# Optimization experiments

Hardware: AMD Instinct MI355X
Metric: run time of the kernel (lower is better)

The kernel has to match this reference:

```python
import jax, jax.numpy as jnp
import numpy as np

N_NODES = 10000
N_EDGES = 160000
IN_CH = 256
HID = 128
HEADS = 8
OUT_CH = 32
NEG_SLOPE = 0.2  # PyG GATv2Conv default


def setup_inputs() -> dict:
    key = jax.random.key(0)
    ks = jax.random.split(key, 12)
    x = jax.random.normal(ks[0], (N_NODES, IN_CH), dtype=jnp.float32)
    edge_index = jax.random.randint(ks[1], (2, N_EDGES), 0, N_NODES, dtype=jnp.int32)
    s1 = 1.0 / np.sqrt(IN_CH)
    s2 = 1.0 / np.sqrt(HEADS * HID)
    return {
        "x": x,
        "edge_index": edge_index,
        # conv1: GATv2Conv(256 -> 128, heads=8, concat=True)
        "W1_l": jax.random.normal(ks[2], (IN_CH, HEADS * HID), dtype=jnp.float32) * s1,
        "W1_r": jax.random.normal(ks[3], (IN_CH, HEADS * HID), dtype=jnp.float32) * s1,
        "att1": jax.random.normal(ks[4], (HEADS, HID), dtype=jnp.float32) * s1,
        "b1": jnp.zeros((HEADS * HID,), dtype=jnp.float32),
        # conv2: GATv2Conv(1024 -> 32, heads=1, concat=False)
        "W2_l": jax.random.normal(ks[5], (HEADS * HID, OUT_CH), dtype=jnp.float32) * s2,
        "W2_r": jax.random.normal(ks[6], (HEADS * HID, OUT_CH), dtype=jnp.float32) * s2,
        "att2": jax.random.normal(ks[7], (1, OUT_CH), dtype=jnp.float32) * s2,
        "b2": jnp.zeros((OUT_CH,), dtype=jnp.float32),
    }


def _gatv2_conv(x, src, dst, W_l, W_r, att, bias, heads, out_ch, concat):
    """PyG GATv2Conv (inference): e_ij = att . LeakyReLU(Wl x_j + Wr x_i),
    segment-softmax over incoming edges per dst node, scatter-add of Wl x_j."""
    n = x.shape[0]
    xl = (x @ W_l).reshape(n, heads, out_ch)  # source transform [N,H,C]
    xr = (x @ W_r).reshape(n, heads, out_ch)  # target transform [N,H,C]
    msg = jax.nn.leaky_relu(xl[src] + xr[dst], NEG_SLOPE)  # [E,H,C]
    e = jnp.einsum('ehc,hc->eh', msg, att)  # [E,H]
    # numerically stable segment softmax over dst
    e_max = jax.ops.segment_max(e, dst, num_segments=n)  # [N,H]
    ex = jnp.exp(e - e_max[dst])
    denom = jax.ops.segment_sum(ex, dst, num_segments=n)  # [N,H]
    alpha = ex / (denom[dst] + 1e-16)  # [E,H]
    out = jax.ops.segment_sum(xl[src] * alpha[:, :, None], dst, num_segments=n)  # [N,H,C]
    if concat:
        out = out.reshape(n, heads * out_ch)
    else:
        out = out.mean(axis=1)
    return out + bias


def reference(x, edge_index, W1_l, W1_r, att1, b1, W2_l, W2_r, att2, b2):
    src, dst = edge_index[0], edge_index[1]
    # dropout is identity in eval mode
    h = _gatv2_conv(x, src, dst, W1_l, W1_r, att1, b1, HEADS, HID, concat=True)
    h = jax.nn.elu(h)
    h = _gatv2_conv(h, src, dst, W2_l, W2_r, att2, b2, 1, OUT_CH, concat=False)
    return jax.nn.log_softmax(h, axis=1)
```

## Files before the change

kernel.cpp:

```cpp
#include <hip/hip_runtime.h>
#include <hip/hip_bf16.h>

constexpr int NN   = 10000;
constexpr int NE   = 160000;
constexpr int INC  = 256;
constexpr int H    = 8;
constexpr int D1   = 1024;
constexpr int OUTC = 32;
constexpr int MPAD = 10112;
constexpr float NEG_SLOPE = 0.2f;

typedef __attribute__((ext_vector_type(8))) short bf16x8;
typedef __attribute__((ext_vector_type(4))) float f32x4;

__device__ __forceinline__ unsigned short f2b(float f) {
  unsigned u = __float_as_uint(f);
  unsigned r = (u + 0x7fffu + ((u >> 16) & 1u)) >> 16;
  return (unsigned short)r;
}
__device__ __forceinline__ float b2f_lo(unsigned u) { return __uint_as_float(u << 16); }
__device__ __forceinline__ float b2f_hi(unsigned u) { return __uint_as_float(u & 0xffff0000u); }
__device__ __forceinline__ float lrelu(float a) { return fmaxf(a, 0.f) + NEG_SLOPE * fminf(a, 0.f); }

constexpr int NB_CVT = MPAD * INC / 4 / 256;
constexpr int NB_W1X = 2048 / 32;
constexpr int NB_W1  = NB_W1X * (256 / 32);
constexpr int NB_W2X = 64 / 32;
constexpr int NB_W2  = NB_W2X * (1024 / 32);
constexpr int NB_DEG = (NE + 255) / 256;

__device__ __forceinline__ void transpose_body(const float* __restrict__ srcA,
                                               const float* __restrict__ srcB,
                                               short* __restrict__ dst,
                                               int K, int NsrcHalf, int bx, int by,
                                               int tx, int ty) {
  __shared__ float tile[32][33];
  int nb = bx * 32, kb = by * 32;
  const float* src = srcA;
  int nloc = nb;
  if (nb >= NsrcHalf) { src = srcB; nloc = nb - NsrcHalf; }
#pragma unroll
  for (int i = 0; i < 4; i++)
    tile[ty + i * 8][tx] = src[(size_t)(kb + ty + i * 8) * NsrcHalf + nloc + tx];
  __syncthreads();
#pragma unroll
  for (int i = 0; i < 4; i++)
    dst[(size_t)(nb + ty + i * 8) * K + kb + tx] = (short)f2b(tile[tx][ty + i * 8]);
}

__global__ __launch_bounds__(256) void prep(const float* __restrict__ x, short* __restrict__ Xb,
                                            const float* __restrict__ W1l, const float* __restrict__ W1r,
                                            short* __restrict__ Wt1,
                                            const float* __restrict__ W2l, const float* __restrict__ W2r,
                                            short* __restrict__ Wt2,
                                            const int* __restrict__ dst, int* __restrict__ deg) {
  const int b = blockIdx.x;
  const int t = threadIdx.x;
  if (b < NB_CVT) {
    int base = (b * 256 + t) * 4;
    ushort4 o;
    if (base < NN * INC) {
      float4 v = *(const float4*)(x + base);
      o.x = f2b(v.x); o.y = f2b(v.y); o.z = f2b(v.z); o.w = f2b(v.w);
    } else {
      o.x = o.y = o.z = o.w = 0;
    }
    *(ushort4*)(Xb + base) = o;
  } else if (b < NB_CVT + NB_W1) {
    int bb = b - NB_CVT;
    transpose_body(W1l, W1r, Wt1, 256, 1024, bb % NB_W1X, bb / NB_W1X, t & 31, t >> 5);
  } else if (b < NB_CVT + NB_W1 + NB_W2) {
    int bb = b - NB_CVT - NB_W1;
    transpose_body(W2l, W2r, Wt2, 1024, 32, bb % NB_W2X, bb / NB_W2X, t & 31, t >> 5);
  } else {
    int e = (b - NB_CVT - NB_W1 - NB_W2) * 256 + t;
    if (e < NE) atomicAdd(&deg[dst[e]], 1);
  }
}

__global__ __launch_bounds__(1024) void scan_rowptr(const int* __restrict__ deg,
                                                    int* __restrict__ rowptr,
                                                    int* __restrict__ cursor) {
  __shared__ int wsum[16];
  const int t = threadIdx.x;
  const int lane = t & 63, w = t >> 6;
  const int base = t * 10;
  int v[10];
  int tot = 0;
#pragma unroll
  for (int i = 0; i < 10; i++) {
    int idx = base + i;
    int x = (idx < NN) ? deg[idx] : 0;
    v[i] = tot;
    tot += x;
  }
  int ws = tot;
#pragma unroll
  for (int off = 1; off < 64; off <<= 1) {
    int u = __shfl_up(ws, off);
    if (lane >= off) ws += u;
  }
  if (lane == 63) wsum[w] = ws;
  __syncthreads();
  if (w == 0) {
    int x = (lane < 16) ? wsum[lane] : 0;
#pragma unroll
    for (int off = 1; off < 16; off <<= 1) {
      int u = __shfl_up(x, off);
      if (lane >= off) x += u;
    }
    if (lane < 16) wsum[lane] = x;
  }
  __syncthreads();
  const int wbase = (w > 0) ? wsum[w - 1] : 0;
  const int tbase = wbase + ws - tot;
#pragma unroll
  for (int i = 0; i < 10; i++) {
    int idx = base + i;
    if (idx < NN) {
      int r = tbase + v[i];
      rowptr[idx] = r;
      cursor[idx] = r;
    }
  }
  if (t == 1023) rowptr[NN] = wbase + ws;
}

__global__ void csr_fill(const int* __restrict__ src, const int* __restrict__ dst,
                         int* __restrict__ cursor, int* __restrict__ csr_s) {
  int e = blockIdx.x * 256 + threadIdx.x;
  if (e >= NE) return;
  int pos = atomicAdd(&cursor[dst[e]], 1);
  csr_s[pos] = src[e];
}

__global__ __launch_bounds__(256) void gemm1_fused(const short* __restrict__ Xb,
                                                   const short* __restrict__ Wt,
                                                   const float* __restrict__ att,
                                                   short* __restrict__ xlr,
                                                   float* __restrict__ alar) {
  __shared__ short As[4096];
  __shared__ short Bs[4096];
  __shared__ short Cs[128][136];
  const int t = threadIdx.x;
  const int lane = t & 63;
  const int w = t >> 6;
  const int wr = w >> 1, wc = w & 1;
  const int row0 = blockIdx.y * 128;
  const int col0 = blockIdx.x * 128;
  const int r_st = t & 127;
  const int kc_st = t >> 7;
  f32x4 acc[4][4] = {};
  for (int k0 = 0; k0 < 256; k0 += 32) {
    bf16x8 va0 = *(const bf16x8*)(Xb + (size_t)(row0 + r_st) * 256 + k0 + kc_st * 8);
    bf16x8 va1 = *(const bf16x8*)(Xb + (size_t)(row0 + r_st) * 256 + k0 + (kc_st + 2) * 8);
    bf16x8 vb0 = *(const bf16x8*)(Wt + (size_t)(col0 + r_st) * 256 + k0 + kc_st * 8);
    bf16x8 vb1 = *(const bf16x8*)(Wt + (size_t)(col0 + r_st) * 256 + k0 + (kc_st + 2) * 8);
    __syncthreads();
    *(bf16x8*)&As[(kc_st)     * 1024 + r_st * 8] = va0;
    *(bf16x8*)&As[(kc_st + 2) * 1024 + r_st * 8] = va1;
    *(bf16x8*)&Bs[(kc_st)     * 1024 + r_st * 8] = vb0;
    *(bf16x8*)&Bs[(kc_st + 2) * 1024 + r_st * 8] = vb1;
    __syncthreads();
    bf16x8 af[4], bfr[4];
#pragma unroll
    for (int i = 0; i < 4; i++)
      af[i] = *(const bf16x8*)&As[(lane >> 4) * 1024 + (wr * 64 + i * 16 + (lane & 15)) * 8];
#pragma unroll
    for (int j = 0; j < 4; j++)
      bfr[j] = *(const bf16x8*)&Bs[(lane >> 4) * 1024 + (wc * 64 + j * 16 + (lane & 15)) * 8];
#pragma unroll
    for (int i = 0; i < 4; i++)
#pragma unroll
      for (int j = 0; j < 4; j++)
        acc[i][j] = __builtin_amdgcn_mfma_f32_16x16x32_bf16(af[i], bfr[j], acc[i][j], 0, 0, 0);
  }
  __syncthreads();
#pragma unroll
  for (int i = 0; i < 4; i++) {
#pragma unroll
    for (int reg = 0; reg < 4; reg++) {
      int r = wr * 64 + i * 16 + (lane >> 4) * 4 + reg;
#pragma unroll
      for (int j = 0; j < 4; j++)
        Cs[r][wc * 64 + j * 16 + (lane & 15)] = (short)f2b(acc[i][j][reg]);
    }
  }
  __syncthreads();
  const int r = t >> 1, half = t & 1;
  const int gr = row0 + r;
  float dot = 0.f;
  if (gr < NN) {
#pragma unroll
    for (int chunk = 0; chunk < 8; chunk++) {
      const int cloc = half * 64 + chunk * 8;
      uint4 v = *(const uint4*)&Cs[r][cloc];
      *(uint4*)(xlr + (size_t)gr * 2048 + col0 + cloc) = v;
      const int ca = (col0 + cloc) & 1023;
      const float4 a0 = *(const float4*)(att + ca);
      const float4 a1 = *(const float4*)(att + ca + 4);
      dot += b2f_lo(v.x) * a0.x + b2f_hi(v.x) * a0.y
           + b2f_lo(v.y) * a0.z + b2f_hi(v.y) * a0.w
           + b2f_lo(v.z) * a1.x + b2f_hi(v.z) * a1.y
           + b2f_lo(v.w) * a1.z + b2f_hi(v.w) * a1.w;
    }
  }
  dot += __shfl_xor(dot, 1);
  if (half == 0 && gr < NN) alar[gr * 16 + blockIdx.x] = dot;
}

__global__ __launch_bounds__(256) void gemm2_64(const short* __restrict__ h1b,
                                                const short* __restrict__ Wt2,
                                                float* __restrict__ xlr2) {
  __shared__ short As[4][64][8];
  __shared__ short Bs[4][64][8];
  const int t = threadIdx.x;
  const int lane = t & 63;
  const int wv = t >> 6;
  const int wr = wv >> 1, wc = wv & 1;
  const int row0 = blockIdx.y * 64;
  const int r_st = t & 63;
  const int kc2 = t >> 6;
  f32x4 acc[2][2] = {};
  for (int k0 = 0; k0 < 1024; k0 += 32) {
    bf16x8 va = *(const bf16x8*)(h1b + (size_t)(row0 + r_st) * 1024 + k0 + kc2 * 8);
    bf16x8 vb = *(const bf16x8*)(Wt2 + (size_t)r_st * 1024 + k0 + kc2 * 8);
    __syncthreads();
    *(bf16x8*)&As[kc2][r_st][0] = va;
    *(bf16x8*)&Bs[kc2][r_st][0] = vb;
    __syncthreads();
    const int ks = lane >> 4;
    bf16x8 af0 = *(const bf16x8*)&As[ks][wr * 32 + (lane & 15)][0];
    bf16x8 af1 = *(const bf16x8*)&As[ks][wr * 32 + 16 + (lane & 15)][0];
    bf16x8 bf0 = *(const bf16x8*)&Bs[ks][wc * 32 + (lane & 15)][0];
    bf16x8 bf1 = *(const bf16x8*)&Bs[ks][wc * 32 + 16 + (lane & 15)][0];
    acc[0][0] = __builtin_amdgcn_mfma_f32_16x16x32_bf16(af0, bf0, acc[0][0], 0, 0, 0);
    acc[0][1] = __builtin_amdgcn_mfma_f32_16x16x32_bf16(af0, bf1, acc[0][1], 0, 0, 0);
    acc[1][0] = __builtin_amdgcn_mfma_f32_16x16x32_bf16(af1, bf0, acc[1][0], 0, 0, 0);
    acc[1][1] = __builtin_amdgcn_mfma_f32_16x16x32_bf16(af1, bf1, acc[1][1], 0, 0, 0);
  }
#pragma unroll
  for (int i = 0; i < 2; i++) {
#pragma unroll
    for (int reg = 0; reg < 4; reg++) {
      int gr = row0 + wr * 32 + i * 16 + (lane >> 4) * 4 + reg;
      if (gr < NN) {
#pragma unroll
        for (int j = 0; j < 2; j++) {
          int gc = wc * 32 + j * 16 + (lane & 15);
          xlr2[(size_t)gr * 64 + gc] = acc[i][j][reg];
        }
      }
    }
  }
}

__global__ __launch_bounds__(256) void score1n(const int* __restrict__ rowptr, const int* __restrict__ csr_s,
                                               const short* __restrict__ xlr, const float* __restrict__ att,
                                               const float* __restrict__ alar,
                                               float* __restrict__ w1, float* __restrict__ den1) {
  const int lane = threadIdx.x & 63;
  const int d = blockIdx.x * 4 + (threadIdx.x >> 6);
  if (d >= NN) return;
  const int h = lane >> 3;
  const uint4* xrp = (const uint4*)(xlr + (size_t)d * 2048 + 1024 + lane * 16);
  uint4 rA = xrp[0], rB = xrp[1];
  float xr[16];
  xr[0] = b2f_lo(rA.x); xr[1] = b2f_hi(rA.x); xr[2] = b2f_lo(rA.y); xr[3] = b2f_hi(rA.y);
  xr[4] = b2f_lo(rA.z); xr[5] = b2f_hi(rA.z); xr[6] = b2f_lo(rA.w); xr[7] = b2f_hi(rA.w);
  xr[8] = b2f_lo(rB.x); xr[9] = b2f_hi(rB.x); xr[10] = b2f_lo(rB.y); xr[11] = b2f_hi(rB.y);
  xr[12] = b2f_lo(rB.z); xr[13] = b2f_hi(rB.z); xr[14] = b2f_lo(rB.w); xr[15] = b2f_hi(rB.w);
  const float4* a4 = (const float4*)(att + lane * 16);
  const float4 t0 = a4[0], t1 = a4[1], t2 = a4[2], t3 = a4[3];
  const float ar_h = alar[d * 16 + 8 + h];
  const int jb = rowptr[d], je = rowptr[d + 1];
  float den = 0.f;
#pragma unroll 2
  for (int j = jb; j < je; j++) {
    int s = csr_s[j];
    const uint4* xp = (const uint4*)(xlr + (size_t)s * 2048 + lane * 16);
    uint4 A = xp[0], B = xp[1];
    float p;
    p  = fabsf(b2f_lo(A.x) + xr[0]) * t0.x;
    p += fabsf(b2f_hi(A.x) + xr[1]) * t0.y;
    p += fabsf(b2f_lo(A.y) + xr[2]) * t0.z;
    p += fabsf(b2f_hi(A.y) + xr[3]) * t0.w;
    p += fabsf(b2f_lo(A.z) + xr[4]) * t1.x;
    p += fabsf(b2f_hi(A.z) + xr[5]) * t1.y;
    p += fabsf(b2f_lo(A.w) + xr[6]) * t1.z;
    p += fabsf(b2f_hi(A.w) + xr[7]) * t1.w;
    p += fabsf(b2f_lo(B.x) + xr[8]) * t2.x;
    p += fabsf(b2f_hi(B.x) + xr[9]) * t2.y;
    p += fabsf(b2f_lo(B.y) + xr[10]) * t2.z;
    p += fabsf(b2f_hi(B.y) + xr[11]) * t2.w;
    p += fabsf(b2f_lo(B.z) + xr[12]) * t3.x;
    p += fabsf(b2f_hi(B.z) + xr[13]) * t3.y;
    p += fabsf(b2f_lo(B.w) + xr[14]) * t3.z;
    p += fabsf(b2f_hi(B.w) + xr[15]) * t3.w;
    p += __shfl_xor(p, 1);
    p += __shfl_xor(p, 2);
    p += __shfl_xor(p, 4);
    float e = 0.4f * p + 0.6f * (alar[s * 16 + h] + ar_h);
    float w = __expf(e);
    den += w;
    if ((lane & 7) == 0) w1[j * 8 + h] = w;
  }
  if ((lane & 7) == 0) den1[d * 8 + h] = den;
}

__global__ __launch_bounds__(256) void agg1_fast(const int* __restrict__ rowptr, const int* __restrict__ csr_s,
                                                 const float* __restrict__ w1, const float* __restrict__ den1,
                                                 const short* __restrict__ xlr,
                                                 const float* __restrict__ b1, short* __restrict__ h1b) {
  const int widx = threadIdx.x >> 6;
  const int lane = threadIdx.x & 63;
  const int d = blockIdx.x * 2 + (widx >> 1);
  const int ch = (widx & 1) * 512 + lane * 8;
  const int h = ch >> 7;
  const int jb = rowptr[d], je = rowptr[d + 1];
  float a0 = 0.f, a1 = 0.f, a2 = 0.f, a3 = 0.f, a4 = 0.f, a5 = 0.f, a6 = 0.f, a7 = 0.f;
#pragma unroll 4
  for (int j = jb; j < je; j++) {
    int s = csr_s[j];
    float al = w1[j * 8 + h];
    uint4 v = *(const uint4*)(xlr + (size_t)s * 2048 + ch);
    a0 += al * b2f_lo(v.x); a1 += al * b2f_hi(v.x);
    a2 += al * b2f_lo(v.y); a3 += al * b2f_hi(v.y);
    a4 += al * b2f_lo(v.z); a5 += al * b2f_hi(v.z);
    a6 += al * b2f_lo(v.w); a7 += al * b2f_hi(v.w);
  }
  const float inv = 1.f / (den1[d * 8 + h] + 1e-16f);
  const float4 b0 = *(const float4*)(b1 + ch);
  const float4 b4 = *(const float4*)(b1 + ch + 4);
  a0 = a0 * inv + b0.x; a1 = a1 * inv + b0.y; a2 = a2 * inv + b0.z; a3 = a3 * inv + b0.w;
  a4 = a4 * inv + b4.x; a5 = a5 * inv + b4.y; a6 = a6 * inv + b4.z; a7 = a7 * inv + b4.w;
  a0 = a0 > 0.f ? a0 : expm1f(a0);
  a1 = a1 > 0.f ? a1 : expm1f(a1);
  a2 = a2 > 0.f ? a2 : expm1f(a2);
  a3 = a3 > 0.f ? a3 : expm1f(a3);
  a4 = a4 > 0.f ? a4 : expm1f(a4);
  a5 = a5 > 0.f ? a5 : expm1f(a5);
  a6 = a6 > 0.f ? a6 : expm1f(a6);
  a7 = a7 > 0.f ? a7 : expm1f(a7);
  ushort4 o0, o4;
  o0.x = f2b(a0); o0.y = f2b(a1); o0.z = f2b(a2); o0.w = f2b(a3);
  o4.x = f2b(a4); o4.y = f2b(a5); o4.z = f2b(a6); o4.w = f2b(a7);
  *(ushort4*)(h1b + (size_t)d * 1024 + ch) = o0;
  *(ushort4*)(h1b + (size_t)d * 1024 + ch + 4) = o4;
}

__global__ __launch_bounds__(256) void score2n(const int* __restrict__ rowptr, const int* __restrict__ csr_s,
                                               const float* __restrict__ xlr2, const float* __restrict__ att2,
                                               float* __restrict__ w2, float* __restrict__ den2) {
  const int t = threadIdx.x;
  const int d = blockIdx.x * 8 + (t >> 5);
  const int c = t & 31;
  if (d >= NN) return;
  const float xr = xlr2[d * 64 + 32 + c];
  const float a2 = att2[c];
  const int jb = rowptr[d], je = rowptr[d + 1];
  float den = 0.f;
#pragma unroll 2
  for (int j = jb; j < je; j++) {
    int s = csr_s[j];
    float p = a2 * lrelu(xlr2[s * 64 + c] + xr);
#pragma unroll
    for (int off = 16; off > 0; off >>= 1) p += __shfl_xor(p, off);
    float w = __expf(p);
    den += w;
    if (c == 0) w2[j] = w;
  }
  if (c == 0) den2[d] = den;
}

__global__ __launch_bounds__(256) void agg2_fast(const int* __restrict__ rowptr, const int* __restrict__ csr_s,
                                                 const float* __restrict__ w2, const float* __restrict__ den2,
                                                 const float* __restrict__ xlr2,
                                                 const float* __restrict__ b2, float* __restrict__ out) {
  const int t = threadIdx.x;
  const int d = blockIdx.x * 8 + (t >> 5);
  const int c = t & 31;
  if (d >= NN) return;
  const int jb = rowptr[d], je = rowptr[d + 1];
  float acc = 0.f;
#pragma unroll 4
  for (int j = jb; j < je; j++) {
    acc += w2[j] * xlr2[csr_s[j] * 64 + c];
  }
  const float inv = 1.f / (den2[d] + 1e-16f);
  float v = acc * inv + b2[c];
  float mx = v;
#pragma unroll
  for (int off = 16; off > 0; off >>= 1) mx = fmaxf(mx, __shfl_xor(mx, off));
  float ex = __expf(v - mx);
  float sum = ex;
#pragma unroll
  for (int off = 16; off > 0; off >>= 1) sum += __shfl_xor(sum, off);
  out[d * 32 + c] = v - mx - logf(sum);
}

extern "C" void kernel_launch(void* const* d_in, const int* in_sizes, int n_in,
                              void* d_out, int out_size, void* d_ws, size_t ws_size,
                              hipStream_t stream) {
  const float* x    = (const float*)d_in[0];
  const int*   ei   = (const int*)d_in[1];
  const float* W1l  = (const float*)d_in[2];
  const float* W1r  = (const float*)d_in[3];
  const float* att1 = (const float*)d_in[4];
  const float* b1   = (const float*)d_in[5];
  const float* W2l  = (const float*)d_in[6];
  const float* W2r  = (const float*)d_in[7];
  const float* att2 = (const float*)d_in[8];
  const float* b2   = (const float*)d_in[9];
  float* out = (float*)d_out;

  short* Xb   = (short*)d_ws;
  short* Wt1  = Xb + (size_t)MPAD * 256;
  short* Wt2  = Wt1 + (size_t)2048 * 256;
  short* xlr  = Wt2 + (size_t)64 * 1024;
  short* h1b  = xlr + (size_t)NN * 2048;
  float* xlr2 = (float*)(h1b + (size_t)MPAD * 1024);
  float* alar = xlr2 + (size_t)NN * 64;
  float* w1   = alar + (size_t)NN * 16;
  float* den1 = w1 + (size_t)NE * 8;
  float* w2   = den1 + (size_t)NN * 8;
  float* den2 = w2 + NE;
  int* deg    = (int*)(den2 + NN);
  int* rowptr = deg + NN;
  int* cursor = rowptr + NN + 1;
  int* csr_s  = cursor + NN;

  const int* src = ei;
  const int* dst = ei + NE;

  hipMemsetAsync(deg, 0, NN * sizeof(int), stream);
  prep<<<NB_CVT + NB_W1 + NB_W2 + NB_DEG, 256, 0, stream>>>(x, Xb, W1l, W1r, Wt1,
                                                            W2l, W2r, Wt2, dst, deg);
  scan_rowptr<<<1, 1024, 0, stream>>>(deg, rowptr, cursor);
  csr_fill<<<(NE + 255) / 256, 256, 0, stream>>>(src, dst, cursor, csr_s);

  {
    dim3 g(16, 79);
    gemm1_fused<<<g, 256, 0, stream>>>(Xb, Wt1, att1, xlr, alar);
  }

  score1n<<<(NN + 3) / 4, 256, 0, stream>>>(rowptr, csr_s, xlr, att1, alar, w1, den1);
  agg1_fast<<<NN / 2, 256, 0, stream>>>(rowptr, csr_s, w1, den1, xlr, b1, h1b);

  {
    dim3 g(1, MPAD / 64);
    gemm2_64<<<g, 256, 0, stream>>>(h1b, Wt2, xlr2);
  }

  score2n<<<(NN + 7) / 8, 256, 0, stream>>>(rowptr, csr_s, xlr2, att2, w2, den2);
  agg2_fast<<<(NN + 7) / 8, 256, 0, stream>>>(rowptr, csr_s, w2, den2, xlr2, b2, out);
}
```

Measured before the change: 299.4 us.

## Fuse attention scoring and aggregation with online softmax for both GAT layers

Merges the score and aggregate kernels of each GATv2 layer into one kernel that computes edge scores and accumulates weighted source features in one pass, using an online-softmax running max with rescaling. This removes the intermediate edge-weight and denominator buffers and the second gather of source features per edge. In exchange, layer 1 now reduces scores across 16 lanes per head instead of 8, and the conditional rescale adds branches and extra exps inside the edge loop. The layer-1 loop also loses its unroll pragma.

```diff
diff --git a/kernel.cpp b/kernel.cpp
--- a/kernel.cpp
+++ b/kernel.cpp
@@ -255,103 +255,82 @@
   }
 }
 
-__global__ __launch_bounds__(256) void score1n(const int* __restrict__ rowptr, const int* __restrict__ csr_s,
-                                               const short* __restrict__ xlr, const float* __restrict__ att,
-                                               const float* __restrict__ alar,
-                                               float* __restrict__ w1, float* __restrict__ den1) {
-  const int lane = threadIdx.x & 63;
-  const int d = blockIdx.x * 4 + (threadIdx.x >> 6);
-  if (d >= NN) return;
-  const int h = lane >> 3;
-  const uint4* xrp = (const uint4*)(xlr + (size_t)d * 2048 + 1024 + lane * 16);
-  uint4 rA = xrp[0], rB = xrp[1];
-  float xr[16];
-  xr[0] = b2f_lo(rA.x); xr[1] = b2f_hi(rA.x); xr[2] = b2f_lo(rA.y); xr[3] = b2f_hi(rA.y);
-  xr[4] = b2f_lo(rA.z); xr[5] = b2f_hi(rA.z); xr[6] = b2f_lo(rA.w); xr[7] = b2f_hi(rA.w);
-  xr[8] = b2f_lo(rB.x); xr[9] = b2f_hi(rB.x); xr[10] = b2f_lo(rB.y); xr[11] = b2f_hi(rB.y);
-  xr[12] = b2f_lo(rB.z); xr[13] = b2f_hi(rB.z); xr[14] = b2f_lo(rB.w); xr[15] = b2f_hi(rB.w);
-  const float4* a4 = (const float4*)(att + lane * 16);
-  const float4 t0 = a4[0], t1 = a4[1], t2 = a4[2], t3 = a4[3];
-  const float ar_h = alar[d * 16 + 8 + h];
-  const int jb = rowptr[d], je = rowptr[d + 1];
-  float den = 0.f;
-#pragma unroll 2
-  for (int j = jb; j < je; j++) {
-    int s = csr_s[j];
-    const uint4* xp = (const uint4*)(xlr + (size_t)s * 2048 + lane * 16);
-    uint4 A = xp[0], B = xp[1];
-    float p;
-    p  = fabsf(b2f_lo(A.x) + xr[0]) * t0.x;
-    p += fabsf(b2f_hi(A.x) + xr[1]) * t0.y;
-    p += fabsf(b2f_lo(A.y) + xr[2]) * t0.z;
-    p += fabsf(b2f_hi(A.y) + xr[3]) * t0.w;
-    p += fabsf(b2f_lo(A.z) + xr[4]) * t1.x;
-    p += fabsf(b2f_hi(A.z) + xr[5]) * t1.y;
-    p += fabsf(b2f_lo(A.w) + xr[6]) * t1.z;
-    p += fabsf(b2f_hi(A.w) + xr[7]) * t1.w;
-    p += fabsf(b2f_lo(B.x) + xr[8]) * t2.x;
-    p += fabsf(b2f_hi(B.x) + xr[9]) * t2.y;
-    p += fabsf(b2f_lo(B.y) + xr[10]) * t2.z;
-    p += fabsf(b2f_hi(B.y) + xr[11]) * t2.w;
-    p += fabsf(b2f_lo(B.z) + xr[12]) * t3.x;
-    p += fabsf(b2f_hi(B.z) + xr[13]) * t3.y;
-    p += fabsf(b2f_lo(B.w) + xr[14]) * t3.z;
-    p += fabsf(b2f_hi(B.w) + xr[15]) * t3.w;
-    p += __shfl_xor(p, 1);
-    p += __shfl_xor(p, 2);
-    p += __shfl_xor(p, 4);
-    float e = 0.4f * p + 0.6f * (alar[s * 16 + h] + ar_h);
-    float w = __expf(e);
-    den += w;
-    if ((lane & 7) == 0) w1[j * 8 + h] = w;
-  }
-  if ((lane & 7) == 0) den1[d * 8 + h] = den;
-}
-
-__global__ __launch_bounds__(256) void agg1_fast(const int* __restrict__ rowptr, const int* __restrict__ csr_s,
-                                                 const float* __restrict__ w1, const float* __restrict__ den1,
-                                                 const short* __restrict__ xlr,
-                                                 const float* __restrict__ b1, short* __restrict__ h1b) {
+__global__ __launch_bounds__(256) void fused1(const int* __restrict__ rowptr, const int* __restrict__ csr_s,
+                                              const short* __restrict__ xlr, const float* __restrict__ att,
+                                              const float* __restrict__ alar,
+                                              const float* __restrict__ b1, short* __restrict__ h1b) {
   const int widx = threadIdx.x >> 6;
   const int lane = threadIdx.x & 63;
   const int d = blockIdx.x * 2 + (widx >> 1);
   const int ch = (widx & 1) * 512 + lane * 8;
   const int h = ch >> 7;
+  const uint4 rv = *(const uint4*)(xlr + (size_t)d * 2048 + 1024 + ch);
+  const float xr0 = b2f_lo(rv.x), xr1 = b2f_hi(rv.x);
+  const float xr2 = b2f_lo(rv.y), xr3 = b2f_hi(rv.y);
+  const float xr4 = b2f_lo(rv.z), xr5 = b2f_hi(rv.z);
+  const float xr6 = b2f_lo(rv.w), xr7 = b2f_hi(rv.w);
+  const float4 ta = *(const float4*)(att + ch);
+  const float4 tb = *(const float4*)(att + ch + 4);
+  const float ar_h = alar[d * 16 + 8 + h];
   const int jb = rowptr[d], je = rowptr[d + 1];
-  float a0 = 0.f, a1 = 0.f, a2 = 0.f, a3 = 0.f, a4 = 0.f, a5 = 0.f, a6 = 0.f, a7 = 0.f;
-#pragma unroll 4
+  float m = -3.4e38f, den = 0.f;
+  float c0 = 0.f, c1 = 0.f, c2 = 0.f, c3 = 0.f, c4 = 0.f, c5 = 0.f, c6 = 0.f, c7 = 0.f;
   for (int j = jb; j < je; j++) {
-    int s = csr_s[j];
-    float al = w1[j * 8 + h];
-    uint4 v = *(const uint4*)(xlr + (size_t)s * 2048 + ch);
-    a0 += al * b2f_lo(v.x); a1 += al * b2f_hi(v.x);
-    a2 += al * b2f_lo(v.y); a3 += al * b2f_hi(v.y);
-    a4 += al * b2f_lo(v.z); a5 += al * b2f_hi(v.z);
-    a6 += al * b2f_lo(v.w); a7 += al * b2f_hi(v.w);
-  }
-  const float inv = 1.f / (den1[d * 8 + h] + 1e-16f);
+    const int s = csr_s[j];
+    const uint4 v = *(const uint4*)(xlr + (size_t)s * 2048 + ch);
+    const float x0 = b2f_lo(v.x), x1 = b2f_hi(v.x);
+    const float x2 = b2f_lo(v.y), x3 = b2f_hi(v.y);
+    const float x4 = b2f_lo(v.z), x5 = b2f_hi(v.z);
+    const float x6 = b2f_lo(v.w), x7 = b2f_hi(v.w);
+    float p = fabsf(x0 + xr0) * ta.x;
+    p += fabsf(x1 + xr1) * ta.y;
+    p += fabsf(x2 + xr2) * ta.z;
+    p += fabsf(x3 + xr3) * ta.w;
+    p += fabsf(x4 + xr4) * tb.x;
+    p += fabsf(x5 + xr5) * tb.y;
+    p += fabsf(x6 + xr6) * tb.z;
+    p += fabsf(x7 + xr7) * tb.w;
+    p += __shfl_xor(p, 1);
+    p += __shfl_xor(p, 2);
+    p += __shfl_xor(p, 4);
+    p += __shfl_xor(p, 8);
+    const float e = 0.4f * p + 0.6f * (alar[s * 16 + h] + ar_h);
+    if (e > m) {
+      const float r = __expf(m - e);
+      c0 *= r; c1 *= r; c2 *= r; c3 *= r;
+      c4 *= r; c5 *= r; c6 *= r; c7 *= r;
+      den *= r;
+      m = e;
+    }
+    const float w = __expf(e - m);
+    den += w;
+    c0 += w * x0; c1 += w * x1; c2 += w * x2; c3 += w * x3;
+    c4 += w * x4; c5 += w * x5; c6 += w * x6; c7 += w * x7;
+  }
+  const float inv = 1.f / (den + 1e-16f);
   const float4 b0 = *(const float4*)(b1 + ch);
   const float4 b4 = *(const float4*)(b1 + ch + 4);
-  a0 = a0 * inv + b0.x; a1 = a1 * inv + b0.y; a2 = a2 * inv + b0.z; a3 = a3 * inv + b0.w;
-  a4 = a4 * inv + b4.x; a5 = a5 * inv + b4.y; a6 = a6 * inv + b4.z; a7 = a7 * inv + b4.w;
-  a0 = a0 > 0.f ? a0 : expm1f(a0);
-  a1 = a1 > 0.f ? a1 : expm1f(a1);
-  a2 = a2 > 0.f ? a2 : expm1f(a2);
-  a3 = a3 > 0.f ? a3 : expm1f(a3);
-  a4 = a4 > 0.f ? a4 : expm1f(a4);
-  a5 = a5 > 0.f ? a5 : expm1f(a5);
-  a6 = a6 > 0.f ? a6 : expm1f(a6);
-  a7 = a7 > 0.f ? a7 : expm1f(a7);
-  ushort4 o0, o4;
-  o0.x = f2b(a0); o0.y = f2b(a1); o0.z = f2b(a2); o0.w = f2b(a3);
-  o4.x = f2b(a4); o4.y = f2b(a5); o4.z = f2b(a6); o4.w = f2b(a7);
-  *(ushort4*)(h1b + (size_t)d * 1024 + ch) = o0;
-  *(ushort4*)(h1b + (size_t)d * 1024 + ch + 4) = o4;
-}
-
-__global__ __launch_bounds__(256) void score2n(const int* __restrict__ rowptr, const int* __restrict__ csr_s,
-                                               const float* __restrict__ xlr2, const float* __restrict__ att2,
-                                               float* __restrict__ w2, float* __restrict__ den2) {
+  c0 = c0 * inv + b0.x; c1 = c1 * inv + b0.y; c2 = c2 * inv + b0.z; c3 = c3 * inv + b0.w;
+  c4 = c4 * inv + b4.x; c5 = c5 * inv + b4.y; c6 = c6 * inv + b4.z; c7 = c7 * inv + b4.w;
+  c0 = c0 > 0.f ? c0 : expm1f(c0);
+  c1 = c1 > 0.f ? c1 : expm1f(c1);
+  c2 = c2 > 0.f ? c2 : expm1f(c2);
+  c3 = c3 > 0.f ? c3 : expm1f(c3);
+  c4 = c4 > 0.f ? c4 : expm1f(c4);
+  c5 = c5 > 0.f ? c5 : expm1f(c5);
+  c6 = c6 > 0.f ? c6 : expm1f(c6);
+  c7 = c7 > 0.f ? c7 : expm1f(c7);
+  uint4 o;
+  o.x = (unsigned)f2b(c0) | ((unsigned)f2b(c1) << 16);
+  o.y = (unsigned)f2b(c2) | ((unsigned)f2b(c3) << 16);
+  o.z = (unsigned)f2b(c4) | ((unsigned)f2b(c5) << 16);
+  o.w = (unsigned)f2b(c6) | ((unsigned)f2b(c7) << 16);
+  *(uint4*)(h1b + (size_t)d * 1024 + ch) = o;
+}
+
+__global__ __launch_bounds__(256) void fused2(const int* __restrict__ rowptr, const int* __restrict__ csr_s,
+                                              const float* __restrict__ xlr2, const float* __restrict__ att2,
+                                              const float* __restrict__ b2, float* __restrict__ out) {
   const int t = threadIdx.x;
   const int d = blockIdx.x * 8 + (t >> 5);
   const int c = t & 31;
@@ -359,36 +338,22 @@
   const float xr = xlr2[d * 64 + 32 + c];
   const float a2 = att2[c];
   const int jb = rowptr[d], je = rowptr[d + 1];
-  float den = 0.f;
-#pragma unroll 2
+  float m = -3.4e38f, den = 0.f, acc = 0.f;
   for (int j = jb; j < je; j++) {
-    int s = csr_s[j];
-    float p = a2 * lrelu(xlr2[s * 64 + c] + xr);
+    const int s = csr_s[j];
+    const float xv = xlr2[s * 64 + c];
+    float p = a2 * lrelu(xv + xr);
 #pragma unroll
     for (int off = 16; off > 0; off >>= 1) p += __shfl_xor(p, off);
-    float w = __expf(p);
+    if (p > m) {
+      const float r = __expf(m - p);
+      acc *= r; den *= r; m = p;
+    }
+    const float w = __expf(p - m);
     den += w;
-    if (c == 0) w2[j] = w;
-  }
-  if (c == 0) den2[d] = den;
-}
-
-__global__ __launch_bounds__(256) void agg2_fast(const int* __restrict__ rowptr, const int* __restrict__ csr_s,
-                                                 const float* __restrict__ w2, const float* __restrict__ den2,
-                                                 const float* __restrict__ xlr2,
-                                                 const float* __restrict__ b2, float* __restrict__ out) {
-  const int t = threadIdx.x;
-  const int d = blockIdx.x * 8 + (t >> 5);
-  const int c = t & 31;
-  if (d >= NN) return;
-  const int jb = rowptr[d], je = rowptr[d + 1];
-  float acc = 0.f;
-#pragma unroll 4
-  for (int j = jb; j < je; j++) {
-    acc += w2[j] * xlr2[csr_s[j] * 64 + c];
-  }
-  const float inv = 1.f / (den2[d] + 1e-16f);
-  float v = acc * inv + b2[c];
+    acc += w * xv;
+  }
+  float v = acc / (den + 1e-16f) + b2[c];
   float mx = v;
 #pragma unroll
   for (int off = 16; off > 0; off >>= 1) mx = fmaxf(mx, __shfl_xor(mx, off));
@@ -421,11 +386,7 @@
   short* h1b  = xlr + (size_t)NN * 2048;
   float* xlr2 = (float*)(h1b + (size_t)MPAD * 1024);
   float* alar = xlr2 + (size_t)NN * 64;
-  float* w1   = alar + (size_t)NN * 16;
-  float* den1 = w1 + (size_t)NE * 8;
-  float* w2   = den1 + (size_t)NN * 8;
-  float* den2 = w2 + NE;
-  int* deg    = (int*)(den2 + NN);
+  int* deg    = (int*)(alar + (size_t)NN * 16);
   int* rowptr = deg + NN;
   int* cursor = rowptr + NN + 1;
   int* csr_s  = cursor + NN;
@@ -444,14 +405,12 @@
     gemm1_fused<<<g, 256, 0, stream>>>(Xb, Wt1, att1, xlr, alar);
   }
 
-  score1n<<<(NN + 3) / 4, 256, 0, stream>>>(rowptr, csr_s, xlr, att1, alar, w1, den1);
-  agg1_fast<<<NN / 2, 256, 0, stream>>>(rowptr, csr_s, w1, den1, xlr, b1, h1b);
+  fused1<<<NN / 2, 256, 0, stream>>>(rowptr, csr_s, xlr, att1, alar, b1, h1b);
 
   {
     dim3 g(1, MPAD / 64);
     gemm2_64<<<g, 256, 0, stream>>>(h1b, Wt2, xlr2);
   }
 
-  score2n<<<(NN + 7) / 8, 256, 0, stream>>>(rowptr, csr_s, xlr2, att2, w2, den2);
-  agg2_fast<<<(NN + 7) / 8, 256, 0, stream>>>(rowptr, csr_s, w2, den2, xlr2, b2, out);
-}
+  fused2<<<(NN + 7) / 8, 256, 0, stream>>>(rowptr, csr_s, xlr2, att2, b2, out);
+}
```

New measurement: 259.0 us. 1.16x faster.
